# Kernel tuning notes

Measured on AMD Instinct MI355X. Metric: run time of the kernel, lower is better.

Reference implementation:

```python
import jax, jax.numpy as jnp
import numpy as np

B, T, D, U = 32, 1024, 512, 512

def hard_sigmoid(x):
    # Keras hard_sigmoid: clip(0.2*x + 0.5, 0, 1)
    return jnp.clip(x * 0.2 + 0.5, 0.0, 1.0)

def setup_inputs() -> dict:
    key = jax.random.key(0)
    k1, k2, k3 = jax.random.split(key, 3)
    x = jax.random.normal(k1, (B, T, D), dtype=jnp.float32)
    kernel = jax.random.normal(k2, (D, 4 * U), dtype=jnp.float32) * 0.02
    recurrent_kernel = jax.random.normal(k3, (U, 4 * U), dtype=jnp.float32) * 0.02
    # unit_forget_bias: forget-gate slice initialized to 1
    bias = jnp.zeros((4 * U,), dtype=jnp.float32).at[U:2 * U].set(1.0)
    return {"x": x, "kernel": kernel, "recurrent_kernel": recurrent_kernel, "bias": bias}

def reference(x, kernel, recurrent_kernel, bias):
    units = recurrent_kernel.shape[0]
    batch = x.shape[0]
    # Precompute input projections for all timesteps in one big GEMM
    # (implementation=2 style): [B, T, 4U]
    xz = jnp.einsum('btd,dg->btg', x, kernel) + bias
    xz_t = jnp.transpose(xz, (1, 0, 2))  # [T, B, 4U]

    h0 = jnp.zeros((batch, units), dtype=x.dtype)
    c0 = jnp.zeros((batch, units), dtype=x.dtype)

    def step(carry, z_x):
        h, c = carry
        z = z_x + h @ recurrent_kernel  # [B, 4U]
        zi, zf, zc, zo = jnp.split(z, 4, axis=-1)
        i = hard_sigmoid(zi)
        f = hard_sigmoid(zf)
        c_new = f * c + i * jnp.tanh(zc)
        o = hard_sigmoid(zo)
        h_new = o * jnp.tanh(c_new)
        return (h_new, c_new), h_new

    (_, _), hs = jax.lax.scan(step, (h0, c0), xz_t)  # hs: [T, B, U]
    return jnp.transpose(hs, (1, 0, 2))  # [B, T, U] (return_sequences=True)
```

## Files before the change

### kernel.cpp

```cpp
#include <hip/hip_runtime.h>


#define TT 1024
#define DD 512
#define UU 512
#define NCOL 2048
#define SENT 0xFFFFFFFFu
#define RDEPTH 4

__device__ __forceinline__ float hsig(float v) {
  return fminf(fmaxf(0.2f * v + 0.5f, 0.0f), 1.0f);
}
__device__ __forceinline__ float tanh_fast(float x) {
  float e = __expf(2.0f * x);
  return 1.0f - 2.0f / (e + 1.0f);
}

__device__ __forceinline__ void dot64x2_4(
    const float* p0, const float* p1, const float* p2, const float* p3,
    const float (&W)[128],
    float& a00, float& a01, float& a10, float& a11,
    float& a20, float& a21, float& a30, float& a31) {
  a00 = a01 = a10 = a11 = a20 = a21 = a30 = a31 = 0.f;
#pragma unroll
  for (int j4 = 0; j4 < 16; ++j4) {
    float4 v0 = *(const float4*)(p0 + j4 * 4);
    float4 v1 = *(const float4*)(p1 + j4 * 4);
    float4 v2 = *(const float4*)(p2 + j4 * 4);
    float4 v3 = *(const float4*)(p3 + j4 * 4);
    const float* e0 = (const float*)&v0;
    const float* e1 = (const float*)&v1;
    const float* e2 = (const float*)&v2;
    const float* e3 = (const float*)&v3;
#pragma unroll
    for (int jj = 0; jj < 4; ++jj) {
      float w0 = W[2 * (4 * j4 + jj) + 0];
      float w1 = W[2 * (4 * j4 + jj) + 1];
      a00 += e0[jj] * w0; a01 += e0[jj] * w1;
      a10 += e1[jj] * w0; a11 += e1[jj] * w1;
      a20 += e2[jj] * w0; a21 += e2[jj] * w1;
      a30 += e3[jj] * w0; a31 += e3[jj] * w1;
    }
  }
}

__device__ __forceinline__ void wavebar(int* ctr, int& ep) {
  asm volatile("s_waitcnt lgkmcnt(0)" ::: "memory");
  if ((threadIdx.x & 63) == 0)
    __hip_atomic_fetch_add(ctr, 1, __ATOMIC_RELAXED, __HIP_MEMORY_SCOPE_WORKGROUP);
  ep += 4;
  while (__hip_atomic_load(ctr, __ATOMIC_RELAXED, __HIP_MEMORY_SCOPE_WORKGROUP) < ep) {
  }
  asm volatile("" ::: "memory");
}

__global__ __launch_bounds__(512, 2) void lstm_persistent(
    const float* __restrict__ x,
    const float* __restrict__ Wk,
    const float* __restrict__ Wr,
    const float* __restrict__ bias,
    float* __restrict__ out) {
  const int tid = (int)threadIdx.x;
  const int g   = (int)blockIdx.x & 7;
  const int w   = (int)blockIdx.x >> 3;
  const bool crit = (tid < 256);
  const int idx = tid & 255;
  const int o   = idx >> 5;
  const int col0 = (idx & 31) * 2;
  const int gcol = ((col0 >> 4) * UU) + w * 16 + (col0 & 15);

  const float* M = crit ? Wr : Wk;
  float W[128];
#pragma unroll
  for (int j = 0; j < 64; ++j) {
    float2 ww = *(const float2*)(M + (size_t)(o * 64 + j) * NCOL + gcol);
    W[2 * j] = ww.x; W[2 * j + 1] = ww.y;
  }

  __shared__ float LX[8][4][65];
  __shared__ float LR[8][4][65];
  __shared__ float RING[RDEPTH][4][66];
  __shared__ float LH[4][512];
  __shared__ float LB[64];
  __shared__ int cXZdone, cCRITdone, cXZbar, cCRITbar;

  if (tid == 0) { cXZdone = 0; cCRITdone = 0; cXZbar = 0; cCRITbar = 0; }
  if (tid < 64) LB[tid] = bias[(tid >> 4) * UU + w * 16 + (tid & 15)];
  __syncthreads();

  if (crit) {
    const unsigned* ou0 = (const unsigned*)out + (size_t)(g * 4 + 0) * TT * UU;
    const unsigned* ou1 = (const unsigned*)out + (size_t)(g * 4 + 1) * TT * UU;
    const unsigned* ou2 = (const unsigned*)out + (size_t)(g * 4 + 2) * TT * UU;
    const unsigned* ou3 = (const unsigned*)out + (size_t)(g * 4 + 3) * TT * UU;
    const int b_own = tid >> 4;
    const int u_own = tid & 15;
    float c_state = 0.0f;
    int epC = 0;

    for (int t = 0; t < TT; ++t) {
      if (t > 0) {
        size_t roff = (size_t)(t - 1) * UU;
        unsigned v0, v1, v2, v3, v4, v5, v6, v7;
        for (;;) {
          v0 = __hip_atomic_load(ou0 + roff + idx,       __ATOMIC_RELAXED, __HIP_MEMORY_SCOPE_AGENT);
          v1 = __hip_atomic_load(ou0 + roff + idx + 256, __ATOMIC_RELAXED, __HIP_MEMORY_SCOPE_AGENT);
          v2 = __hip_atomic_load(ou1 + roff + idx,       __ATOMIC_RELAXED, __HIP_MEMORY_SCOPE_AGENT);
          v3 = __hip_atomic_load(ou1 + roff + idx + 256, __ATOMIC_RELAXED, __HIP_MEMORY_SCOPE_AGENT);
          v4 = __hip_atomic_load(ou2 + roff + idx,       __ATOMIC_RELAXED, __HIP_MEMORY_SCOPE_AGENT);
          v5 = __hip_atomic_load(ou2 + roff + idx + 256, __ATOMIC_RELAXED, __HIP_MEMORY_SCOPE_AGENT);
          v6 = __hip_atomic_load(ou3 + roff + idx,       __ATOMIC_RELAXED, __HIP_MEMORY_SCOPE_AGENT);
          v7 = __hip_atomic_load(ou3 + roff + idx + 256, __ATOMIC_RELAXED, __HIP_MEMORY_SCOPE_AGENT);
          int ok = (v0 != SENT) & (v1 != SENT) & (v2 != SENT) & (v3 != SENT) &
                   (v4 != SENT) & (v5 != SENT) & (v6 != SENT) & (v7 != SENT);
          if (__all(ok)) break;
          __builtin_amdgcn_s_sleep(1);
        }
        LH[0][idx]       = __uint_as_float(v0);
        LH[0][idx + 256] = __uint_as_float(v1);
        LH[1][idx]       = __uint_as_float(v2);
        LH[1][idx + 256] = __uint_as_float(v3);
        LH[2][idx]       = __uint_as_float(v4);
        LH[2][idx + 256] = __uint_as_float(v5);
        LH[3][idx]       = __uint_as_float(v6);
        LH[3][idx + 256] = __uint_as_float(v7);
      }
      wavebar(&cCRITbar, epC);
      if (t > 0) {
        __builtin_amdgcn_s_setprio(1);
        float a00,a01,a10,a11,a20,a21,a30,a31;
        dot64x2_4(&LH[0][o * 64], &LH[1][o * 64], &LH[2][o * 64], &LH[3][o * 64],
                  W, a00,a01,a10,a11,a20,a21,a30,a31);
        *(float2*)&LR[o][0][col0] = make_float2(a00, a01);
        *(float2*)&LR[o][1][col0] = make_float2(a10, a11);
        *(float2*)&LR[o][2][col0] = make_float2(a20, a21);
        *(float2*)&LR[o][3][col0] = make_float2(a30, a31);
        __builtin_amdgcn_s_setprio(0);
      }
      wavebar(&cCRITbar, epC);
      if (tid < 64) {
        while (__hip_atomic_load(&cXZdone, __ATOMIC_RELAXED,
                                 __HIP_MEMORY_SCOPE_WORKGROUP) < t + 1) {
        }
        asm volatile("" ::: "memory");
        const int s = t & (RDEPTH - 1);
        float s0 = RING[s][b_own][u_own +  0] + LB[u_own +  0];
        float s1 = RING[s][b_own][u_own + 16] + LB[u_own + 16];
        float s2 = RING[s][b_own][u_own + 32] + LB[u_own + 32];
        float s3 = RING[s][b_own][u_own + 48] + LB[u_own + 48];
        if (t > 0) {
#pragma unroll
          for (int oo = 0; oo < 8; ++oo) {
            s0 += LR[oo][b_own][u_own +  0];
            s1 += LR[oo][b_own][u_own + 16];
            s2 += LR[oo][b_own][u_own + 32];
            s3 += LR[oo][b_own][u_own + 48];
          }
        }
        float gi = hsig(s0);
        float gf = hsig(s1);
        float gc = tanh_fast(s2);
        float go = hsig(s3);
        c_state = gf * c_state + gi * gc;
        float h = go * tanh_fast(c_state);
        __hip_atomic_store(
            out + ((size_t)(g * 4 + b_own) * TT + t) * UU + w * 16 + u_own, h,
            __ATOMIC_RELAXED, __HIP_MEMORY_SCOPE_AGENT);
      }
      if (tid == 0) {
        asm volatile("s_waitcnt lgkmcnt(0)" ::: "memory");
        __hip_atomic_fetch_add(&cCRITdone, 1, __ATOMIC_RELAXED,
                               __HIP_MEMORY_SCOPE_WORKGROUP);
      }
    }
  } else {
    const float* xb0 = x + (size_t)(g * 4 + 0) * TT * DD + o * 64;
    const float* xb1 = x + (size_t)(g * 4 + 1) * TT * DD + o * 64;
    const float* xb2 = x + (size_t)(g * 4 + 2) * TT * DD + o * 64;
    const float* xb3 = x + (size_t)(g * 4 + 3) * TT * DD + o * 64;
    int epX = 0;

    for (int t = 0; t < TT; ++t) {
      size_t off = (size_t)t * DD;
      float a00,a01,a10,a11,a20,a21,a30,a31;
      dot64x2_4(xb0 + off, xb1 + off, xb2 + off, xb3 + off, W,
                a00,a01,a10,a11,a20,a21,a30,a31);
      *(float2*)&LX[o][0][col0] = make_float2(a00, a01);
      *(float2*)&LX[o][1][col0] = make_float2(a10, a11);
      *(float2*)&LX[o][2][col0] = make_float2(a20, a21);
      *(float2*)&LX[o][3][col0] = make_float2(a30, a31);
      wavebar(&cXZbar, epX);
      if (t >= RDEPTH) {
        while (__hip_atomic_load(&cCRITdone, __ATOMIC_RELAXED,
                                 __HIP_MEMORY_SCOPE_WORKGROUP) < t - RDEPTH + 1) {
          __builtin_amdgcn_s_sleep(1);
        }
        asm volatile("" ::: "memory");
      }
      {
        const int b2 = idx >> 6, c3 = idx & 63;
        float ssum = 0.f;
#pragma unroll
        for (int oo = 0; oo < 8; ++oo) ssum += LX[oo][b2][c3];
        RING[t & (RDEPTH - 1)][b2][c3] = ssum;
      }
      wavebar(&cXZbar, epX);
      if (idx == 0) {
        asm volatile("s_waitcnt lgkmcnt(0)" ::: "memory");
        __hip_atomic_fetch_add(&cXZdone, 1, __ATOMIC_RELAXED,
                               __HIP_MEMORY_SCOPE_WORKGROUP);
      }
    }
  }
}

extern "C" void kernel_launch(void* const* d_in, const int* in_sizes, int n_in,
                              void* d_out, int out_size, void* d_ws, size_t ws_size,
                              hipStream_t stream) {
  const float* x    = (const float*)d_in[0];
  const float* Wk   = (const float*)d_in[1];
  const float* Wr   = (const float*)d_in[2];
  const float* bias = (const float*)d_in[3];
  float* out = (float*)d_out;

  hipMemsetAsync(out, 0xFF, (size_t)out_size * sizeof(float), stream);
  lstm_persistent<<<256, 512, 0, stream>>>(x, Wk, Wr, bias, out);
}
```

Measured before the change: 4.620 ms.

## Drop one workgroup barrier per step using wave-local h loads and double-buffered LR

Each critical wave now loads only the 128-unit slice of the previous hidden state that its own dot product reads, so the wave-wide barrier between filling LH and the recurrent GEMV is removed. The LR partial-sum buffer is double-buffered by timestep parity so the next step's writes cannot clobber values the gate-update wave is still reading. The xz producer waves also sleep while spinning in their barrier to free issue slots for the critical path. This relies on the wave-to-slice mapping matching the dot64 column ownership, and the double buffering depends on the single remaining barrier for ordering.

```diff
diff --git a/kernel.cpp b/kernel.cpp
--- a/kernel.cpp
+++ b/kernel.cpp
@@ -44,12 +44,14 @@
   }
 }
 
+template <bool SLEEP>
 __device__ __forceinline__ void wavebar(int* ctr, int& ep) {
   asm volatile("s_waitcnt lgkmcnt(0)" ::: "memory");
   if ((threadIdx.x & 63) == 0)
     __hip_atomic_fetch_add(ctr, 1, __ATOMIC_RELAXED, __HIP_MEMORY_SCOPE_WORKGROUP);
   ep += 4;
   while (__hip_atomic_load(ctr, __ATOMIC_RELAXED, __HIP_MEMORY_SCOPE_WORKGROUP) < ep) {
+    if (SLEEP) __builtin_amdgcn_s_sleep(1);
   }
   asm volatile("" ::: "memory");
 }
@@ -78,7 +80,7 @@
   }
 
   __shared__ float LX[8][4][65];
-  __shared__ float LR[8][4][65];
+  __shared__ float LR[2][8][4][65];
   __shared__ float RING[RDEPTH][4][66];
   __shared__ float LH[4][512];
   __shared__ float LB[64];
@@ -89,6 +91,8 @@
   __syncthreads();
 
   if (crit) {
+    const int wv = tid >> 6;
+    const int l  = tid & 63;
     const unsigned* ou0 = (const unsigned*)out + (size_t)(g * 4 + 0) * TT * UU;
     const unsigned* ou1 = (const unsigned*)out + (size_t)(g * 4 + 1) * TT * UU;
     const unsigned* ou2 = (const unsigned*)out + (size_t)(g * 4 + 2) * TT * UU;
@@ -100,44 +104,45 @@
 
     for (int t = 0; t < TT; ++t) {
       if (t > 0) {
-        size_t roff = (size_t)(t - 1) * UU;
+        const size_t roff = (size_t)(t - 1) * UU + 128 * wv + l;
         unsigned v0, v1, v2, v3, v4, v5, v6, v7;
         for (;;) {
-          v0 = __hip_atomic_load(ou0 + roff + idx,       __ATOMIC_RELAXED, __HIP_MEMORY_SCOPE_AGENT);
-          v1 = __hip_atomic_load(ou0 + roff + idx + 256, __ATOMIC_RELAXED, __HIP_MEMORY_SCOPE_AGENT);
-          v2 = __hip_atomic_load(ou1 + roff + idx,       __ATOMIC_RELAXED, __HIP_MEMORY_SCOPE_AGENT);
-          v3 = __hip_atomic_load(ou1 + roff + idx + 256, __ATOMIC_RELAXED, __HIP_MEMORY_SCOPE_AGENT);
-          v4 = __hip_atomic_load(ou2 + roff + idx,       __ATOMIC_RELAXED, __HIP_MEMORY_SCOPE_AGENT);
-          v5 = __hip_atomic_load(ou2 + roff + idx + 256, __ATOMIC_RELAXED, __HIP_MEMORY_SCOPE_AGENT);
-          v6 = __hip_atomic_load(ou3 + roff + idx,       __ATOMIC_RELAXED, __HIP_MEMORY_SCOPE_AGENT);
-          v7 = __hip_atomic_load(ou3 + roff + idx + 256, __ATOMIC_RELAXED, __HIP_MEMORY_SCOPE_AGENT);
+          v0 = __hip_atomic_load(ou0 + roff,      __ATOMIC_RELAXED, __HIP_MEMORY_SCOPE_AGENT);
+          v1 = __hip_atomic_load(ou0 + roff + 64, __ATOMIC_RELAXED, __HIP_MEMORY_SCOPE_AGENT);
+          v2 = __hip_atomic_load(ou1 + roff,      __ATOMIC_RELAXED, __HIP_MEMORY_SCOPE_AGENT);
+          v3 = __hip_atomic_load(ou1 + roff + 64, __ATOMIC_RELAXED, __HIP_MEMORY_SCOPE_AGENT);
+          v4 = __hip_atomic_load(ou2 + roff,      __ATOMIC_RELAXED, __HIP_MEMORY_SCOPE_AGENT);
+          v5 = __hip_atomic_load(ou2 + roff + 64, __ATOMIC_RELAXED, __HIP_MEMORY_SCOPE_AGENT);
+          v6 = __hip_atomic_load(ou3 + roff,      __ATOMIC_RELAXED, __HIP_MEMORY_SCOPE_AGENT);
+          v7 = __hip_atomic_load(ou3 + roff + 64, __ATOMIC_RELAXED, __HIP_MEMORY_SCOPE_AGENT);
           int ok = (v0 != SENT) & (v1 != SENT) & (v2 != SENT) & (v3 != SENT) &
                    (v4 != SENT) & (v5 != SENT) & (v6 != SENT) & (v7 != SENT);
           if (__all(ok)) break;
           __builtin_amdgcn_s_sleep(1);
         }
-        LH[0][idx]       = __uint_as_float(v0);
-        LH[0][idx + 256] = __uint_as_float(v1);
-        LH[1][idx]       = __uint_as_float(v2);
-        LH[1][idx + 256] = __uint_as_float(v3);
-        LH[2][idx]       = __uint_as_float(v4);
-        LH[2][idx + 256] = __uint_as_float(v5);
-        LH[3][idx]       = __uint_as_float(v6);
-        LH[3][idx + 256] = __uint_as_float(v7);
-      }
-      wavebar(&cCRITbar, epC);
-      if (t > 0) {
+        const int ub = 128 * wv + l;
+        LH[0][ub]      = __uint_as_float(v0);
+        LH[0][ub + 64] = __uint_as_float(v1);
+        LH[1][ub]      = __uint_as_float(v2);
+        LH[1][ub + 64] = __uint_as_float(v3);
+        LH[2][ub]      = __uint_as_float(v4);
+        LH[2][ub + 64] = __uint_as_float(v5);
+        LH[3][ub]      = __uint_as_float(v6);
+        LH[3][ub + 64] = __uint_as_float(v7);
+        asm volatile("s_waitcnt lgkmcnt(0)" ::: "memory");
+        __builtin_amdgcn_sched_barrier(0);
         __builtin_amdgcn_s_setprio(1);
         float a00,a01,a10,a11,a20,a21,a30,a31;
         dot64x2_4(&LH[0][o * 64], &LH[1][o * 64], &LH[2][o * 64], &LH[3][o * 64],
                   W, a00,a01,a10,a11,a20,a21,a30,a31);
-        *(float2*)&LR[o][0][col0] = make_float2(a00, a01);
-        *(float2*)&LR[o][1][col0] = make_float2(a10, a11);
-        *(float2*)&LR[o][2][col0] = make_float2(a20, a21);
-        *(float2*)&LR[o][3][col0] = make_float2(a30, a31);
+        const int p = t & 1;
+        *(float2*)&LR[p][o][0][col0] = make_float2(a00, a01);
+        *(float2*)&LR[p][o][1][col0] = make_float2(a10, a11);
+        *(float2*)&LR[p][o][2][col0] = make_float2(a20, a21);
+        *(float2*)&LR[p][o][3][col0] = make_float2(a30, a31);
         __builtin_amdgcn_s_setprio(0);
       }
-      wavebar(&cCRITbar, epC);
+      wavebar<false>(&cCRITbar, epC);
       if (tid < 64) {
         while (__hip_atomic_load(&cXZdone, __ATOMIC_RELAXED,
                                  __HIP_MEMORY_SCOPE_WORKGROUP) < t + 1) {
@@ -149,12 +154,13 @@
         float s2 = RING[s][b_own][u_own + 32] + LB[u_own + 32];
         float s3 = RING[s][b_own][u_own + 48] + LB[u_own + 48];
         if (t > 0) {
+          const int p = t & 1;
 #pragma unroll
           for (int oo = 0; oo < 8; ++oo) {
-            s0 += LR[oo][b_own][u_own +  0];
-            s1 += LR[oo][b_own][u_own + 16];
-            s2 += LR[oo][b_own][u_own + 32];
-            s3 += LR[oo][b_own][u_own + 48];
+            s0 += LR[p][oo][b_own][u_own +  0];
+            s1 += LR[p][oo][b_own][u_own + 16];
+            s2 += LR[p][oo][b_own][u_own + 32];
+            s3 += LR[p][oo][b_own][u_own + 48];
           }
         }
         float gi = hsig(s0);
@@ -189,7 +195,7 @@
       *(float2*)&LX[o][1][col0] = make_float2(a10, a11);
       *(float2*)&LX[o][2][col0] = make_float2(a20, a21);
       *(float2*)&LX[o][3][col0] = make_float2(a30, a31);
-      wavebar(&cXZbar, epX);
+      wavebar<true>(&cXZbar, epX);
       if (t >= RDEPTH) {
         while (__hip_atomic_load(&cCRITdone, __ATOMIC_RELAXED,
                                  __HIP_MEMORY_SCOPE_WORKGROUP) < t - RDEPTH + 1) {
@@ -204,7 +210,7 @@
         for (int oo = 0; oo < 8; ++oo) ssum += LX[oo][b2][c3];
         RING[t & (RDEPTH - 1)][b2][c3] = ssum;
       }
-      wavebar(&cXZbar, epX);
+      wavebar<true>(&cXZbar, epX);
       if (idx == 0) {
         asm volatile("s_waitcnt lgkmcnt(0)" ::: "memory");
         __hip_atomic_fetch_add(&cXZdone, 1, __ATOMIC_RELAXED,
```

Measured after the change: 4.650 ms. Within noise of the previous version (+0.6%).
